# Performance work log

Measured on AMD Instinct MI355X. Metric: run time of the kernel, lower is better.

The kernel has to match this reference:

```python
import jax, jax.numpy as jnp
import numpy as np

N_NODES = 100000
N_EDGES = 1200000
IN_CH = 64


def setup_inputs() -> dict:
    key = jax.random.key(0)
    ks = jax.random.split(key, 6)
    scale = 1.0 / np.sqrt(IN_CH)
    return {
        "x": jax.random.normal(ks[0], (N_NODES, IN_CH), dtype=jnp.float32),
        "edge_index": jax.random.randint(ks[1], (2, N_EDGES), 0, N_NODES, dtype=jnp.int64),
        "W_gcn": jax.random.normal(ks[2], (IN_CH, IN_CH), dtype=jnp.float32) * scale,
        "b_gcn": jnp.zeros((IN_CH,), dtype=jnp.float32),
        "W1": jax.random.normal(ks[3], (IN_CH, 32), dtype=jnp.float32) * scale,
        "b1": jnp.zeros((32,), dtype=jnp.float32),
        "W2": jax.random.normal(ks[4], (32, 32), dtype=jnp.float32) * (1.0 / np.sqrt(32)),
        "b2": jnp.zeros((32,), dtype=jnp.float32),
        "W3": jax.random.normal(ks[5], (32, 2), dtype=jnp.float32) * (1.0 / np.sqrt(32)),
        "b3": jnp.zeros((2,), dtype=jnp.float32),
    }


def _gcn_conv(x, edge_index, W, b):
    # PyG GCNConv: add self-loops, symmetric normalization D^-1/2 A D^-1/2 (X W) + b
    N = x.shape[0]
    loop = jnp.arange(N, dtype=edge_index.dtype)
    src = jnp.concatenate([edge_index[0], loop])
    dst = jnp.concatenate([edge_index[1], loop])
    deg = jax.ops.segment_sum(jnp.ones_like(dst, dtype=x.dtype), dst, num_segments=N)
    d_inv_sqrt = jax.lax.rsqrt(deg)  # deg >= 1 thanks to self-loops
    norm = d_inv_sqrt[src] * d_inv_sqrt[dst]  # [E+N]
    h = x @ W  # [N, C]
    msg = h[src] * norm[:, None]  # gather + scale, [E+N, C]
    agg = jax.ops.segment_sum(msg, dst, num_segments=N)  # scatter-add, [N, C]
    return agg + b


def reference(x, edge_index, W_gcn, b_gcn, W1, b1, W2, b2, W3, b3):
    out = jax.nn.relu(_gcn_conv(x, edge_index, W_gcn, b_gcn))
    h = out + x  # residual
    h = jax.nn.relu(h @ W1 + b1)
    h = jax.nn.relu(h @ W2 + b2)
    return h @ W3 + b3  # [N, 2]
```

## Files before the change

kernel.cpp:

```cpp
#include <hip/hip_runtime.h>

#define NN 100000
#define CH 64
#define CAP 64
#define NPART 8
#define PSIZE ((NN + NPART - 1) / NPART)
#define FILLB 640

__device__ __forceinline__ float bf_lo(unsigned u) { return __uint_as_float(u << 16); }
__device__ __forceinline__ float bf_hi(unsigned u) { return __uint_as_float(u & 0xffff0000u); }

__device__ __forceinline__ unsigned short f2bf(float f) {
    unsigned u = __float_as_uint(f);
    u += 0x7fffu + ((u >> 16) & 1u);
    return (unsigned short)(u >> 16);
}

__global__ __launch_bounds__(256) void k_fill(const int* __restrict__ src,
                                              const int* __restrict__ dst,
                                              unsigned* __restrict__ cnt,
                                              int* __restrict__ bsrc, int E) {
    int part = blockIdx.x & (NPART - 1);
    int blk  = blockIdx.x >> 3;
    int lo = part * PSIZE, hi = lo + PSIZE;
    int E4 = E >> 2;
    const int4* src4 = (const int4*)src;
    const int4* dst4 = (const int4*)dst;
    for (int i = blk * 256 + threadIdx.x; i < E4; i += FILLB * 256) {
        int4 d4 = dst4[i];
        int4 s4 = src4[i];
        if (d4.x >= lo && d4.x < hi) { unsigned p = atomicAdd(&cnt[d4.x], 1u); if (p < CAP) bsrc[(size_t)d4.x * CAP + p] = s4.x; }
        if (d4.y >= lo && d4.y < hi) { unsigned p = atomicAdd(&cnt[d4.y], 1u); if (p < CAP) bsrc[(size_t)d4.y * CAP + p] = s4.y; }
        if (d4.z >= lo && d4.z < hi) { unsigned p = atomicAdd(&cnt[d4.z], 1u); if (p < CAP) bsrc[(size_t)d4.z * CAP + p] = s4.z; }
        if (d4.w >= lo && d4.w < hi) { unsigned p = atomicAdd(&cnt[d4.w], 1u); if (p < CAP) bsrc[(size_t)d4.w * CAP + p] = s4.w; }
    }
    if (part == 0 && blk == 0) {
        for (int e = E4 * 4 + threadIdx.x; e < E; e += 256) {
            int d = dst[e];
            int s = src[e];
            unsigned p = atomicAdd(&cnt[d], 1u);
            if (p < CAP) bsrc[(size_t)d * CAP + p] = s;
        }
    }
}

__global__ __launch_bounds__(256) void k_prep(const float* __restrict__ x,
                                              unsigned short* __restrict__ xb,
                                              const unsigned* __restrict__ cnt,
                                              float* __restrict__ dinv, int N) {
    int i = blockIdx.x * blockDim.x + threadIdx.x;
    int tot4 = N * CH / 4;
    if (i < tot4) {
        float4 v = ((const float4*)x)[i];
        ushort4 o;
        o.x = f2bf(v.x); o.y = f2bf(v.y); o.z = f2bf(v.z); o.w = f2bf(v.w);
        ((ushort4*)xb)[i] = o;
    }
    if (i < N) dinv[i] = rsqrtf((float)cnt[i] + 1.0f);
}

__global__ __launch_bounds__(256) void k_at(
        const unsigned* __restrict__ cnt, const int* __restrict__ bsrc,
        const float* __restrict__ dinv, const float* __restrict__ x,
        const unsigned short* __restrict__ xb,
        const float* __restrict__ Wg, const float* __restrict__ bgcn,
        const float* __restrict__ W1, const float* __restrict__ b1,
        const float* __restrict__ W2, const float* __restrict__ b2,
        const float* __restrict__ W3, const float* __restrict__ b3,
        float* __restrict__ out, int N) {
    __shared__ float R1[4096];
    __shared__ float R2[64 * 65];
    __shared__ float R3[64 * 33];
    __shared__ float bgs[64];
    int t = threadIdx.x;
    int nbase = blockIdx.x * 64;

    for (int i = t; i < 4096; i += 256) R1[i] = Wg[i];
    if (t < 64) bgs[t] = bgcn[t];

    {
        int nl = t >> 2, q = t & 3;
        int n = nbase + nl;
        float* r2p = R2 + nl * 65 + q * 16;
        if (n < N) {
            int c = (int)cnt[n]; if (c > CAP) c = CAP;
            const int* bp = bsrc + (size_t)n * CAP;
            float dn = dinv[n];
            float acc[16];
#pragma unroll
            for (int j = 0; j < 16; ++j) acc[j] = 0.f;
#pragma unroll 2
            for (int e = 0; e < c; ++e) {
                int s = bp[e];
                float w = dinv[s];
                const uint4* xp = (const uint4*)(xb + (size_t)s * CH) + q * 2;
                uint4 A = xp[0], B = xp[1];
                acc[0]  += bf_lo(A.x) * w; acc[1]  += bf_hi(A.x) * w;
                acc[2]  += bf_lo(A.y) * w; acc[3]  += bf_hi(A.y) * w;
                acc[4]  += bf_lo(A.z) * w; acc[5]  += bf_hi(A.z) * w;
                acc[6]  += bf_lo(A.w) * w; acc[7]  += bf_hi(A.w) * w;
                acc[8]  += bf_lo(B.x) * w; acc[9]  += bf_hi(B.x) * w;
                acc[10] += bf_lo(B.y) * w; acc[11] += bf_hi(B.y) * w;
                acc[12] += bf_lo(B.z) * w; acc[13] += bf_hi(B.z) * w;
                acc[14] += bf_lo(B.w) * w; acc[15] += bf_hi(B.w) * w;
            }
            const float4* xq = (const float4*)(x + (size_t)n * CH) + q * 4;
            float4 u0 = xq[0], u1 = xq[1], u2 = xq[2], u3 = xq[3];
            r2p[0]  = dn * (acc[0]  + u0.x * dn); r2p[1]  = dn * (acc[1]  + u0.y * dn);
            r2p[2]  = dn * (acc[2]  + u0.z * dn); r2p[3]  = dn * (acc[3]  + u0.w * dn);
            r2p[4]  = dn * (acc[4]  + u1.x * dn); r2p[5]  = dn * (acc[5]  + u1.y * dn);
            r2p[6]  = dn * (acc[6]  + u1.z * dn); r2p[7]  = dn * (acc[7]  + u1.w * dn);
            r2p[8]  = dn * (acc[8]  + u2.x * dn); r2p[9]  = dn * (acc[9]  + u2.y * dn);
            r2p[10] = dn * (acc[10] + u2.z * dn); r2p[11] = dn * (acc[11] + u2.w * dn);
            r2p[12] = dn * (acc[12] + u3.x * dn); r2p[13] = dn * (acc[13] + u3.y * dn);
            r2p[14] = dn * (acc[14] + u3.z * dn); r2p[15] = dn * (acc[15] + u3.w * dn);
        } else {
#pragma unroll
            for (int j = 0; j < 16; ++j) r2p[j] = 0.f;
        }
    }
    __syncthreads();

    int cg = t & 15, ng = t >> 4;
    float accv[4][4];
#pragma unroll
    for (int i = 0; i < 4; ++i)
#pragma unroll
        for (int u = 0; u < 4; ++u) accv[i][u] = 0.f;
    for (int k = 0; k < 64; ++k) {
        float wv0 = R1[k * 64 + cg * 4 + 0];
        float wv1 = R1[k * 64 + cg * 4 + 1];
        float wv2 = R1[k * 64 + cg * 4 + 2];
        float wv3 = R1[k * 64 + cg * 4 + 3];
        float va = R2[(ng * 4 + 0) * 65 + k];
        float vb = R2[(ng * 4 + 1) * 65 + k];
        float vc = R2[(ng * 4 + 2) * 65 + k];
        float vd = R2[(ng * 4 + 3) * 65 + k];
        accv[0][0] += va * wv0; accv[0][1] += va * wv1; accv[0][2] += va * wv2; accv[0][3] += va * wv3;
        accv[1][0] += vb * wv0; accv[1][1] += vb * wv1; accv[1][2] += vb * wv2; accv[1][3] += vb * wv3;
        accv[2][0] += vc * wv0; accv[2][1] += vc * wv1; accv[2][2] += vc * wv2; accv[2][3] += vc * wv3;
        accv[3][0] += vd * wv0; accv[3][1] += vd * wv1; accv[3][2] += vd * wv2; accv[3][3] += vd * wv3;
    }
    __syncthreads();

    for (int i = t; i < 2048; i += 256) R1[i] = W1[i];
    for (int i = t; i < 1024; i += 256) R1[2048 + i] = W2[i];
    if (t < 64) R1[3072 + t] = W3[t];
    if (t < 32) { R1[3136 + t] = b1[t]; R1[3168 + t] = b2[t]; }
    if (t < 2) R1[3200 + t] = b3[t];
#pragma unroll
    for (int i = 0; i < 4; ++i) {
        int nl2 = ng * 4 + i;
        int gr = nbase + nl2;
        float4 xv = make_float4(0.f, 0.f, 0.f, 0.f);
        if (gr < N) xv = *((const float4*)(x + (size_t)gr * CH) + cg);
        float* rp = R2 + nl2 * 65 + cg * 4;
        rp[0] = fmaxf(accv[i][0] + bgs[cg * 4 + 0], 0.f) + xv.x;
        rp[1] = fmaxf(accv[i][1] + bgs[cg * 4 + 1], 0.f) + xv.y;
        rp[2] = fmaxf(accv[i][2] + bgs[cg * 4 + 2], 0.f) + xv.z;
        rp[3] = fmaxf(accv[i][3] + bgs[cg * 4 + 3], 0.f) + xv.w;
    }
    __syncthreads();

    int nl = t & 63, g = t >> 6;
    {
        float a[8];
#pragma unroll
        for (int j = 0; j < 8; ++j) a[j] = R1[3136 + 8 * g + j];
        for (int k = 0; k < 64; ++k) {
            float v = R2[nl * 65 + k];
#pragma unroll
            for (int j = 0; j < 8; ++j)
                a[j] += v * R1[k * 32 + 8 * g + j];
        }
#pragma unroll
        for (int j = 0; j < 8; ++j) R3[nl * 33 + 8 * g + j] = a[j];
    }
    __syncthreads();

    {
        float a[8];
#pragma unroll
        for (int j = 0; j < 8; ++j) a[j] = R1[3168 + 8 * g + j];
        for (int k = 0; k < 32; ++k) {
            float v = fmaxf(R3[nl * 33 + k], 0.0f);
#pragma unroll
            for (int j = 0; j < 8; ++j)
                a[j] += v * R1[2048 + k * 32 + 8 * g + j];
        }
#pragma unroll
        for (int j = 0; j < 8; ++j) R2[nl * 65 + 8 * g + j] = a[j];
    }
    __syncthreads();

    if (t < 128) {
        int nl4 = t >> 1, g4 = t & 1;
        int gr = nbase + nl4;
        if (gr < N) {
            float y = R1[3200 + g4];
#pragma unroll
            for (int k = 0; k < 32; ++k)
                y += fmaxf(R2[nl4 * 65 + k], 0.0f) * R1[3072 + k * 2 + g4];
            out[(size_t)gr * 2 + g4] = y;
        }
    }
}

extern "C" void kernel_launch(void* const* d_in, const int* in_sizes, int n_in,
                              void* d_out, int out_size, void* d_ws, size_t ws_size,
                              hipStream_t stream) {
    const float* x  = (const float*)d_in[0];
    const int*   ei = (const int*)d_in[1];
    const float* Wg = (const float*)d_in[2];
    const float* bg = (const float*)d_in[3];
    const float* W1 = (const float*)d_in[4];
    const float* b1 = (const float*)d_in[5];
    const float* W2 = (const float*)d_in[6];
    const float* b2 = (const float*)d_in[7];
    const float* W3 = (const float*)d_in[8];
    const float* b3 = (const float*)d_in[9];
    float* out = (float*)d_out;

    const int N = NN;
    const int E = in_sizes[1] / 2;
    const int* src = ei;
    const int* dst = ei + E;

    char* base = (char*)d_ws;
    size_t o = 0;
    auto alloc = [&](size_t bytes) { void* p = base + o; o = (o + bytes + 255) & ~(size_t)255; return p; };
    unsigned*       cnt  = (unsigned*)alloc((size_t)N * 4);
    float*          dinv = (float*)alloc((size_t)N * 4);
    int*            bsrc = (int*)alloc((size_t)N * CAP * 4);
    unsigned short* xb   = (unsigned short*)alloc((size_t)N * CH * 2);

    hipMemsetAsync(cnt, 0, (size_t)N * 4, stream);

    k_fill<<<NPART * FILLB, 256, 0, stream>>>(src, dst, cnt, bsrc, E);
    int prep_blocks = (N * CH / 4 + 255) / 256;
    k_prep<<<prep_blocks, 256, 0, stream>>>(x, xb, cnt, dinv, N);
    k_at<<<(N + 63) / 64, 256, 0, stream>>>(cnt, bsrc, dinv, x, xb, Wg, bg,
                                            W1, b1, W2, b2, W3, b3, out, N);
}
```

Baseline: 218.5 us.

## Halve nodes per block and split each node's gather across eight threads

The fused aggregate-plus-MLP kernel now handles 32 nodes per block instead of 64, with 8 threads per node each gathering 8 bf16 channels (one uint4) instead of 4 threads gathering 16. All dense stages are remapped so each thread computes fewer outputs, and several inner loops get unroll pragmas. The goal is more parallelism and memory-level concurrency in the latency-bound neighbor gather, plus more blocks in flight. The cost is twice as many blocks, each reloading the 16 KB GCN weight matrix into shared memory, which doubles weight-load traffic and per-block setup.

```diff
diff --git a/kernel.cpp b/kernel.cpp
--- a/kernel.cpp
+++ b/kernel.cpp
@@ -69,77 +69,65 @@
         const float* __restrict__ W3, const float* __restrict__ b3,
         float* __restrict__ out, int N) {
     __shared__ float R1[4096];
-    __shared__ float R2[64 * 65];
-    __shared__ float R3[64 * 33];
+    __shared__ float R2[32 * 65];
+    __shared__ float R3[32 * 33];
     __shared__ float bgs[64];
     int t = threadIdx.x;
-    int nbase = blockIdx.x * 64;
+    int nbase = blockIdx.x * 32;
 
     for (int i = t; i < 4096; i += 256) R1[i] = Wg[i];
     if (t < 64) bgs[t] = bgcn[t];
 
     {
-        int nl = t >> 2, q = t & 3;
+        int nl = t >> 3, o = t & 7;
         int n = nbase + nl;
-        float* r2p = R2 + nl * 65 + q * 16;
+        float* r2p = R2 + nl * 65 + o * 8;
         if (n < N) {
             int c = (int)cnt[n]; if (c > CAP) c = CAP;
             const int* bp = bsrc + (size_t)n * CAP;
             float dn = dinv[n];
-            float acc[16];
-#pragma unroll
-            for (int j = 0; j < 16; ++j) acc[j] = 0.f;
-#pragma unroll 2
+            float acc[8];
+#pragma unroll
+            for (int j = 0; j < 8; ++j) acc[j] = 0.f;
+#pragma unroll 4
             for (int e = 0; e < c; ++e) {
                 int s = bp[e];
                 float w = dinv[s];
-                const uint4* xp = (const uint4*)(xb + (size_t)s * CH) + q * 2;
-                uint4 A = xp[0], B = xp[1];
-                acc[0]  += bf_lo(A.x) * w; acc[1]  += bf_hi(A.x) * w;
-                acc[2]  += bf_lo(A.y) * w; acc[3]  += bf_hi(A.y) * w;
-                acc[4]  += bf_lo(A.z) * w; acc[5]  += bf_hi(A.z) * w;
-                acc[6]  += bf_lo(A.w) * w; acc[7]  += bf_hi(A.w) * w;
-                acc[8]  += bf_lo(B.x) * w; acc[9]  += bf_hi(B.x) * w;
-                acc[10] += bf_lo(B.y) * w; acc[11] += bf_hi(B.y) * w;
-                acc[12] += bf_lo(B.z) * w; acc[13] += bf_hi(B.z) * w;
-                acc[14] += bf_lo(B.w) * w; acc[15] += bf_hi(B.w) * w;
+                uint4 A = ((const uint4*)(xb + (size_t)s * CH))[o];
+                acc[0] += bf_lo(A.x) * w; acc[1] += bf_hi(A.x) * w;
+                acc[2] += bf_lo(A.y) * w; acc[3] += bf_hi(A.y) * w;
+                acc[4] += bf_lo(A.z) * w; acc[5] += bf_hi(A.z) * w;
+                acc[6] += bf_lo(A.w) * w; acc[7] += bf_hi(A.w) * w;
             }
-            const float4* xq = (const float4*)(x + (size_t)n * CH) + q * 4;
-            float4 u0 = xq[0], u1 = xq[1], u2 = xq[2], u3 = xq[3];
-            r2p[0]  = dn * (acc[0]  + u0.x * dn); r2p[1]  = dn * (acc[1]  + u0.y * dn);
-            r2p[2]  = dn * (acc[2]  + u0.z * dn); r2p[3]  = dn * (acc[3]  + u0.w * dn);
-            r2p[4]  = dn * (acc[4]  + u1.x * dn); r2p[5]  = dn * (acc[5]  + u1.y * dn);
-            r2p[6]  = dn * (acc[6]  + u1.z * dn); r2p[7]  = dn * (acc[7]  + u1.w * dn);
-            r2p[8]  = dn * (acc[8]  + u2.x * dn); r2p[9]  = dn * (acc[9]  + u2.y * dn);
-            r2p[10] = dn * (acc[10] + u2.z * dn); r2p[11] = dn * (acc[11] + u2.w * dn);
-            r2p[12] = dn * (acc[12] + u3.x * dn); r2p[13] = dn * (acc[13] + u3.y * dn);
-            r2p[14] = dn * (acc[14] + u3.z * dn); r2p[15] = dn * (acc[15] + u3.w * dn);
+            const float4* xq = (const float4*)(x + (size_t)n * CH);
+            float4 u0 = xq[2 * o], u1 = xq[2 * o + 1];
+            r2p[0] = dn * (acc[0] + u0.x * dn); r2p[1] = dn * (acc[1] + u0.y * dn);
+            r2p[2] = dn * (acc[2] + u0.z * dn); r2p[3] = dn * (acc[3] + u0.w * dn);
+            r2p[4] = dn * (acc[4] + u1.x * dn); r2p[5] = dn * (acc[5] + u1.y * dn);
+            r2p[6] = dn * (acc[6] + u1.z * dn); r2p[7] = dn * (acc[7] + u1.w * dn);
         } else {
 #pragma unroll
-            for (int j = 0; j < 16; ++j) r2p[j] = 0.f;
+            for (int j = 0; j < 8; ++j) r2p[j] = 0.f;
         }
     }
     __syncthreads();
 
     int cg = t & 15, ng = t >> 4;
-    float accv[4][4];
-#pragma unroll
-    for (int i = 0; i < 4; ++i)
+    float accv[2][4];
+#pragma unroll
+    for (int i = 0; i < 2; ++i)
 #pragma unroll
         for (int u = 0; u < 4; ++u) accv[i][u] = 0.f;
+#pragma unroll 4
     for (int k = 0; k < 64; ++k) {
         float wv0 = R1[k * 64 + cg * 4 + 0];
         float wv1 = R1[k * 64 + cg * 4 + 1];
         float wv2 = R1[k * 64 + cg * 4 + 2];
         float wv3 = R1[k * 64 + cg * 4 + 3];
-        float va = R2[(ng * 4 + 0) * 65 + k];
-        float vb = R2[(ng * 4 + 1) * 65 + k];
-        float vc = R2[(ng * 4 + 2) * 65 + k];
-        float vd = R2[(ng * 4 + 3) * 65 + k];
+        float va = R2[(ng * 2 + 0) * 65 + k];
+        float vb = R2[(ng * 2 + 1) * 65 + k];
         accv[0][0] += va * wv0; accv[0][1] += va * wv1; accv[0][2] += va * wv2; accv[0][3] += va * wv3;
         accv[1][0] += vb * wv0; accv[1][1] += vb * wv1; accv[1][2] += vb * wv2; accv[1][3] += vb * wv3;
-        accv[2][0] += vc * wv0; accv[2][1] += vc * wv1; accv[2][2] += vc * wv2; accv[2][3] += vc * wv3;
-        accv[3][0] += vd * wv0; accv[3][1] += vd * wv1; accv[3][2] += vd * wv2; accv[3][3] += vd * wv3;
     }
     __syncthreads();
 
@@ -149,8 +137,8 @@
     if (t < 32) { R1[3136 + t] = b1[t]; R1[3168 + t] = b2[t]; }
     if (t < 2) R1[3200 + t] = b3[t];
 #pragma unroll
-    for (int i = 0; i < 4; ++i) {
-        int nl2 = ng * 4 + i;
+    for (int i = 0; i < 2; ++i) {
+        int nl2 = ng * 2 + i;
         int gr = nbase + nl2;
         float4 xv = make_float4(0.f, 0.f, 0.f, 0.f);
         if (gr < N) xv = *((const float4*)(x + (size_t)gr * CH) + cg);
@@ -162,38 +150,40 @@
     }
     __syncthreads();
 
-    int nl = t & 63, g = t >> 6;
+    int nl = t & 31, g2 = t >> 5;
     {
-        float a[8];
-#pragma unroll
-        for (int j = 0; j < 8; ++j) a[j] = R1[3136 + 8 * g + j];
+        float a[4];
+#pragma unroll
+        for (int j = 0; j < 4; ++j) a[j] = R1[3136 + 4 * g2 + j];
+#pragma unroll 4
         for (int k = 0; k < 64; ++k) {
             float v = R2[nl * 65 + k];
 #pragma unroll
-            for (int j = 0; j < 8; ++j)
-                a[j] += v * R1[k * 32 + 8 * g + j];
-        }
-#pragma unroll
-        for (int j = 0; j < 8; ++j) R3[nl * 33 + 8 * g + j] = a[j];
+            for (int j = 0; j < 4; ++j)
+                a[j] += v * R1[k * 32 + 4 * g2 + j];
+        }
+#pragma unroll
+        for (int j = 0; j < 4; ++j) R3[nl * 33 + 4 * g2 + j] = a[j];
     }
     __syncthreads();
 
     {
-        float a[8];
-#pragma unroll
-        for (int j = 0; j < 8; ++j) a[j] = R1[3168 + 8 * g + j];
+        float a[4];
+#pragma unroll
+        for (int j = 0; j < 4; ++j) a[j] = R1[3168 + 4 * g2 + j];
+#pragma unroll 4
         for (int k = 0; k < 32; ++k) {
             float v = fmaxf(R3[nl * 33 + k], 0.0f);
 #pragma unroll
-            for (int j = 0; j < 8; ++j)
-                a[j] += v * R1[2048 + k * 32 + 8 * g + j];
-        }
-#pragma unroll
-        for (int j = 0; j < 8; ++j) R2[nl * 65 + 8 * g + j] = a[j];
-    }
-    __syncthreads();
-
-    if (t < 128) {
+            for (int j = 0; j < 4; ++j)
+                a[j] += v * R1[2048 + k * 32 + 4 * g2 + j];
+        }
+#pragma unroll
+        for (int j = 0; j < 4; ++j) R2[nl * 65 + 4 * g2 + j] = a[j];
+    }
+    __syncthreads();
+
+    if (t < 64) {
         int nl4 = t >> 1, g4 = t & 1;
         int gr = nbase + nl4;
         if (gr < N) {
@@ -239,6 +229,6 @@
     k_fill<<<NPART * FILLB, 256, 0, stream>>>(src, dst, cnt, bsrc, E);
     int prep_blocks = (N * CH / 4 + 255) / 256;
     k_prep<<<prep_blocks, 256, 0, stream>>>(x, xb, cnt, dinv, N);
-    k_at<<<(N + 63) / 64, 256, 0, stream>>>(cnt, bsrc, dinv, x, xb, Wg, bg,
+    k_at<<<(N + 31) / 32, 256, 0, stream>>>(cnt, bsrc, dinv, x, xb, Wg, bg,
                                             W1, b1, W2, b2, W3, b3, out, N);
 }
```

Result: faster. 208.1 us (-4.7%).
